# Optimization experiments

Measured on AMD Instinct MI355X. Metric: run time of the kernel, lower is better.

## Reference

```python
import jax, jax.numpy as jnp
import numpy as np

TEMPERATURE = 0.1
NUM_CLASSES = 100
BATCH = 4096
DIM = 128


def setup_inputs() -> dict:
    key = jax.random.key(0)
    k1, k2, k3 = jax.random.split(key, 3)
    centers1 = jax.random.normal(k1, (NUM_CLASSES, DIM), dtype=jnp.float32)
    features = jax.random.normal(k2, (BATCH, 2, DIM), dtype=jnp.float32)
    # contrastive features are typically L2-normalized; harmless and realistic
    centers1 = centers1 / jnp.linalg.norm(centers1, axis=-1, keepdims=True)
    features = features / jnp.linalg.norm(features, axis=-1, keepdims=True)
    targets = jax.random.randint(k3, (BATCH,), 0, NUM_CLASSES, dtype=jnp.int64 if jax.config.jax_enable_x64 else jnp.int32)
    return {"centers1": centers1, "features": features, "targets": targets}


def reference(centers1, features, targets):
    C = centers1.shape[0]          # num classes
    B = features.shape[0]          # batch size
    t = TEMPERATURE

    # targets for [view0; view1; class centers] -> [2B + C]
    tgt = jnp.concatenate([targets, targets, jnp.arange(C, dtype=targets.dtype)])
    # per-class count over all 2B+C target entries (eye(C)[targets].sum(0))
    batch_cls_count = jnp.zeros((C,), jnp.float32).at[tgt].add(1.0)

    # positive mask [2B, 2B+C], zero out self-contrast on the diagonal
    mask = (tgt[: 2 * B, None] == tgt[None, :]).astype(jnp.float32)
    idx = jnp.arange(2 * B)
    logits_mask = jnp.ones((2 * B, 2 * B + C), jnp.float32).at[idx, idx].set(0.0)
    mask = mask * logits_mask

    # stack: [view0 (B), view1 (B), centers (C)] -> [2B+C, D]
    feats = jnp.concatenate([features[:, 0], features[:, 1], centers1], axis=0)

    # logits [2B, 2B+C], stable max-subtract (detached max)
    logits = jnp.matmul(feats[: 2 * B], feats.T) / t
    logits = logits - jax.lax.stop_gradient(jnp.max(logits, axis=1, keepdims=True))

    exp_logits = jnp.exp(logits) * logits_mask
    # per-instance class-balanced weight, minus mask (as in original)
    per_ins_weight = batch_cls_count[tgt][None, :] - mask  # [2B, 2B+C] via broadcast
    exp_logits_sum = jnp.sum(exp_logits / per_ins_weight, axis=1, keepdims=True)

    log_prob = logits - jnp.log(exp_logits_sum)
    mean_log_prob_pos = jnp.sum(mask * log_prob, axis=1) / jnp.sum(mask, axis=1)
    loss = -mean_log_prob_pos
    return loss.reshape(2, B).mean()
```

## Files before the change

kernel.cpp:

```cpp
#include <hip/hip_runtime.h>
#include <math.h>

constexpr int B_   = 4096;
constexpr int C_   = 100;
constexpr int D_   = 128;
constexpr int TWOB = 8192;
constexpr int NJ   = 8292;
constexpr int NJP  = 8320;
constexpr float LOG2E10 = 14.4269504089f;
constexpr float LN2     = 0.6931471805599453f;

typedef __attribute__((ext_vector_type(8))) short short8;
typedef __attribute__((ext_vector_type(4))) float f32x4;


__device__ __forceinline__ const float* feat_row(const float* __restrict__ centers,
                                                 const float* __restrict__ features,
                                                 int idx) {
  if (idx < B_)   return features + (size_t)idx * (2 * D_);
  if (idx < TWOB) return features + (size_t)(idx - B_) * (2 * D_) + D_;
  return centers + (size_t)(idx - TWOB) * D_;
}

__device__ __forceinline__ unsigned short f2bf(float x) {
  unsigned int u = __float_as_uint(x);
  unsigned int r = (u + 0x7FFFu + ((u >> 16) & 1u)) >> 16;
  return (unsigned short)r;
}

__device__ __forceinline__ float bf2f(short s) {
  return __uint_as_float(((unsigned int)(unsigned short)s) << 16);
}

__global__ __launch_bounds__(256)
void tgt_count_kernel(const int* __restrict__ targets, int* __restrict__ cnt,
                      int* __restrict__ tgtAll) {
  int i = blockIdx.x * 256 + threadIdx.x;
  if (i >= NJP) return;
  int jt = (i < B_) ? targets[i]
         : (i < TWOB ? targets[i - B_] : (i < NJ ? i - TWOB : -9));
  tgtAll[i] = jt;
  if (i < B_) atomicAdd(&cnt[jt], 1);
}

__global__ __launch_bounds__(256)
void prep_kernel(const float* __restrict__ centers, const float* __restrict__ features,
                 const int* __restrict__ tgtAll, const int* __restrict__ cnt,
                 unsigned short* __restrict__ fbB, unsigned short* __restrict__ fbA,
                 float4* __restrict__ tbl) {
  int gidx = blockIdx.x * 256 + threadIdx.x;
  if (gidx >= NJP * 32) return;
  int row = gidx >> 5;
  int q   = gidx & 31;
  float4 v = make_float4(0.f, 0.f, 0.f, 0.f);
  if (row < NJ) v = *(const float4*)(feat_row(centers, features, row) + q * 4);
  ushort4 o;
  o.x = f2bf(v.x); o.y = f2bf(v.y); o.z = f2bf(v.z); o.w = f2bf(v.w);
  *(ushort4*)&fbB[(size_t)row * 128 + q * 4] = o;
  if (row < TWOB) {
    ushort4 a;
    a.x = f2bf(v.x * LOG2E10); a.y = f2bf(v.y * LOG2E10);
    a.z = f2bf(v.z * LOG2E10); a.w = f2bf(v.w * LOG2E10);
    *(ushort4*)&fbA[(size_t)row * 128 + q * 4] = a;
  }
  if (q == 0) {
    int jt = tgtAll[row];
    float r0 = 0.f, r1 = 0.f;
    if (jt >= 0) {
      float b = (float)(2 * cnt[jt] + 1);
      r0 = 1.f / b;
      r1 = 1.f / (b - 1.f);
    }
    tbl[row] = make_float4(__int_as_float(jt), r0, r1, 0.f);
  }
}

__global__ __launch_bounds__(256) __attribute__((amdgpu_waves_per_eu(2, 2)))
void bal_mfma(const unsigned short* __restrict__ fbA, const unsigned short* __restrict__ fbB,
              const float4* __restrict__ tbl, float* __restrict__ Eacc,
              float* __restrict__ Sacc) {
  const int t     = threadIdx.x;
  const int lane  = t & 63;
  const int w     = t >> 6;
  const int id    = blockIdx.x;
  const int strip = id & 15;
  const int isup  = id >> 4;
  const int rbase = isup * 256 + w * 64;
  const int lr    = lane & 15;
  const int lh    = lane >> 4;

  const int q0 = strip * 32 + (strip < 8 ? strip : 8);
  const int q1 = q0 + 32 + (strip < 8 ? 1 : 0);

  short8 af[4][4];
  #pragma unroll
  for (int ks = 0; ks < 4; ++ks)
    #pragma unroll
    for (int m = 0; m < 4; ++m)
      af[ks][m] = *(const short8*)&fbA[(size_t)(rbase + m * 16 + lr) * 128 + (ks * 4 + lh) * 8];

  int ti[4][4];
  #pragma unroll
  for (int m = 0; m < 4; ++m)
    #pragma unroll
    for (int g = 0; g < 4; ++g)
      ti[m][g] = __float_as_int(tbl[rbase + m * 16 + lh * 4 + g].x);

  float ep[4][4], ma[4][4];
  #pragma unroll
  for (int m = 0; m < 4; ++m)
    #pragma unroll
    for (int g = 0; g < 4; ++g) { ep[m][g] = 0.f; ma[m][g] = 0.f; }

  short8 bA[4], bB[4];
  float4 tA, tB;

  auto loadQ = [&](int jq, short8 (&b)[4], float4& tb) {
    int jb = jq * 16;
    tb = tbl[jb + lr];
    #pragma unroll
    for (int ks = 0; ks < 4; ++ks)
      b[ks] = *(const short8*)&fbB[(size_t)(jb + lr) * 128 + (ks * 4 + lh) * 8];
  };

  auto computeQ = [&](short8 (&b)[4], float4& tb) {
    f32x4 acc[4];
    #pragma unroll
    for (int m = 0; m < 4; ++m) acc[m] = (f32x4){0.f, 0.f, 0.f, 0.f};
    #pragma unroll
    for (int ks = 0; ks < 4; ++ks)
      #pragma unroll
      for (int m = 0; m < 4; ++m)
        acc[m] = __builtin_amdgcn_mfma_f32_16x16x32_bf16(af[ks][m], b[ks], acc[m], 0, 0, 0);
    int   jtq = __float_as_int(tb.x);
    float r0q = tb.y, r1q = tb.z;
    #pragma unroll
    for (int m = 0; m < 4; ++m)
      #pragma unroll
      for (int g = 0; g < 4; ++g) {
        float a = acc[m][g];
        float e = __builtin_amdgcn_exp2f(a);
        bool eq = (ti[m][g] == jtq);
        ep[m][g] = fmaf(e, eq ? r1q : r0q, ep[m][g]);
        ma[m][g] += eq ? a : 0.f;
      }
  };

  int jq = q0;
  loadQ(q0, bA, tA);
  while (jq + 2 <= q1) {
    loadQ(jq + 1, bB, tB);
    computeQ(bA, tA);
    if (jq + 2 < q1) loadQ(jq + 2, bA, tA);
    computeQ(bB, tB);
    jq += 2;
  }
  if (jq < q1) computeQ(bA, tA);

  #pragma unroll
  for (int mk = 1; mk <= 8; mk <<= 1)
    #pragma unroll
    for (int m = 0; m < 4; ++m)
      #pragma unroll
      for (int g = 0; g < 4; ++g) {
        ep[m][g] += __shfl_xor(ep[m][g], mk, 64);
        ma[m][g] += __shfl_xor(ma[m][g], mk, 64);
      }
  if (lr == 0) {
    #pragma unroll
    for (int m = 0; m < 4; ++m)
      #pragma unroll
      for (int g = 0; g < 4; ++g) {
        int i = rbase + m * 16 + lh * 4 + g;
        atomicAdd(&Eacc[i], ep[m][g]);
        atomicAdd(&Sacc[i], ma[m][g]);
      }
  }
}

__global__ __launch_bounds__(256)
void bal_final(const unsigned short* __restrict__ fbA, const unsigned short* __restrict__ fbB,
               const float4* __restrict__ tbl,
               const float* __restrict__ Eacc, const float* __restrict__ Sacc,
               float* __restrict__ out) {
  int t    = threadIdx.x;
  int row  = blockIdx.x * 64 + (t >> 2);
  int part = t & 3;
  const unsigned short* pa = fbA + (size_t)row * 128 + part * 32;
  const unsigned short* pb = fbB + (size_t)row * 128 + part * 32;
  float4 tb = tbl[row];

  float sA = 0.f;
  #pragma unroll
  for (int q = 0; q < 4; ++q) {
    short8 va = *(const short8*)&pa[q * 8];
    short8 vb = *(const short8*)&pb[q * 8];
    #pragma unroll
    for (int d = 0; d < 8; ++d)
      sA = fmaf(bf2f(va[d]), bf2f(vb[d]), sA);
  }
  sA += __shfl_xor(sA, 1, 64);
  sA += __shfl_xor(sA, 2, 64);

  float r1 = tb.z;
  float ep = Eacc[row] - __builtin_amdgcn_exp2f(sA) * r1;
  float ma = LN2 * (Sacc[row] - sA);
  float li = ma * r1 - logf(ep);
  float local = -li * (1.f / (8192.f * 4.f));

  #pragma unroll
  for (int mk = 1; mk < 64; mk <<= 1) local += __shfl_xor(local, mk, 64);
  if ((t & 63) == 0) atomicAdd(out, local);
}

extern "C" void kernel_launch(void* const* d_in, const int* in_sizes, int n_in,
                              void* d_out, int out_size, void* d_ws, size_t ws_size,
                              hipStream_t stream) {
  const float* centers  = (const float*)d_in[0];
  const float* features = (const float*)d_in[1];
  const int*   targets  = (const int*)d_in[2];

  char* ws = (char*)d_ws;
  int*            cnt    = (int*)ws;
  float*          Eacc   = (float*)(ws + 512);
  float*          Sacc   = (float*)(ws + 33280);
  int*            tgtAll = (int*)(ws + 66048);
  float4*         tbl    = (float4*)(ws + 99328);
  unsigned short* fbB    = (unsigned short*)(ws + 232448);
  unsigned short* fbA    = (unsigned short*)(ws + 2362368);
  float* out = (float*)d_out;

  hipMemsetAsync(ws, 0, 66048, stream);
  hipMemsetAsync(d_out, 0, sizeof(float), stream);
  tgt_count_kernel<<<(NJP + 255) / 256, 256, 0, stream>>>(targets, cnt, tgtAll);
  prep_kernel<<<(NJP * 32 + 255) / 256, 256, 0, stream>>>(centers, features, tgtAll, cnt,
                                                          fbB, fbA, tbl);
  bal_mfma<<<512, 256, 0, stream>>>(fbA, fbB, tbl, Eacc, Sacc);
  bal_final<<<TWOB / 64, 256, 0, stream>>>(fbA, fbB, tbl, Eacc, Sacc, out);
}
```

Baseline: 120.6 us.

## Replace atomics and memsets with per-strip partials and single-block reductions

After: 214.0 us. 1.78x slower.

```diff
diff --git a/kernel.cpp b/kernel.cpp
--- a/kernel.cpp
+++ b/kernel.cpp
@@ -3,7 +3,6 @@
 
 constexpr int B_   = 4096;
 constexpr int C_   = 100;
-constexpr int D_   = 128;
 constexpr int TWOB = 8192;
 constexpr int NJ   = 8292;
 constexpr int NJP  = 8320;
@@ -17,9 +16,9 @@
 __device__ __forceinline__ const float* feat_row(const float* __restrict__ centers,
                                                  const float* __restrict__ features,
                                                  int idx) {
-  if (idx < B_)   return features + (size_t)idx * (2 * D_);
-  if (idx < TWOB) return features + (size_t)(idx - B_) * (2 * D_) + D_;
-  return centers + (size_t)(idx - TWOB) * D_;
+  if (idx < B_)   return features + (size_t)idx * 256;
+  if (idx < TWOB) return features + (size_t)(idx - B_) * 256 + 128;
+  return centers + (size_t)(idx - TWOB) * 128;
 }
 
 __device__ __forceinline__ unsigned short f2bf(float x) {
@@ -32,15 +31,21 @@
   return __uint_as_float(((unsigned int)(unsigned short)s) << 16);
 }
 
-__global__ __launch_bounds__(256)
+__global__ __launch_bounds__(1024)
 void tgt_count_kernel(const int* __restrict__ targets, int* __restrict__ cnt,
                       int* __restrict__ tgtAll) {
-  int i = blockIdx.x * 256 + threadIdx.x;
-  if (i >= NJP) return;
-  int jt = (i < B_) ? targets[i]
-         : (i < TWOB ? targets[i - B_] : (i < NJ ? i - TWOB : -9));
-  tgtAll[i] = jt;
-  if (i < B_) atomicAdd(&cnt[jt], 1);
+  __shared__ int h[128];
+  int t = threadIdx.x;
+  if (t < 128) h[t] = 0;
+  __syncthreads();
+  for (int i = t; i < NJP; i += 1024) {
+    int jt = (i < B_) ? targets[i]
+           : (i < TWOB ? targets[i - B_] : (i < NJ ? i - TWOB : -9));
+    tgtAll[i] = jt;
+    if (i < B_) atomicAdd(&h[jt], 1);
+  }
+  __syncthreads();
+  if (t < 128) cnt[t] = h[t];
 }
 
 __global__ __launch_bounds__(256)
@@ -75,40 +80,40 @@
   }
 }
 
-__global__ __launch_bounds__(256) __attribute__((amdgpu_waves_per_eu(2, 2)))
+__global__ __launch_bounds__(256, 4)
 void bal_mfma(const unsigned short* __restrict__ fbA, const unsigned short* __restrict__ fbB,
-              const float4* __restrict__ tbl, float* __restrict__ Eacc,
-              float* __restrict__ Sacc) {
+              const float4* __restrict__ tbl,
+              float* __restrict__ Epart, float* __restrict__ Spart) {
   const int t     = threadIdx.x;
   const int lane  = t & 63;
   const int w     = t >> 6;
   const int id    = blockIdx.x;
   const int strip = id & 15;
   const int isup  = id >> 4;
-  const int rbase = isup * 256 + w * 64;
+  const int rbase = isup * 128 + w * 32;
   const int lr    = lane & 15;
   const int lh    = lane >> 4;
 
   const int q0 = strip * 32 + (strip < 8 ? strip : 8);
   const int q1 = q0 + 32 + (strip < 8 ? 1 : 0);
 
-  short8 af[4][4];
+  short8 af[4][2];
   #pragma unroll
   for (int ks = 0; ks < 4; ++ks)
     #pragma unroll
-    for (int m = 0; m < 4; ++m)
+    for (int m = 0; m < 2; ++m)
       af[ks][m] = *(const short8*)&fbA[(size_t)(rbase + m * 16 + lr) * 128 + (ks * 4 + lh) * 8];
 
-  int ti[4][4];
-  #pragma unroll
-  for (int m = 0; m < 4; ++m)
+  int ti[2][4];
+  #pragma unroll
+  for (int m = 0; m < 2; ++m)
     #pragma unroll
     for (int g = 0; g < 4; ++g)
       ti[m][g] = __float_as_int(tbl[rbase + m * 16 + lh * 4 + g].x);
 
-  float ep[4][4], ma[4][4];
-  #pragma unroll
-  for (int m = 0; m < 4; ++m)
+  float ep[2][4], ma[2][4];
+  #pragma unroll
+  for (int m = 0; m < 2; ++m)
     #pragma unroll
     for (int g = 0; g < 4; ++g) { ep[m][g] = 0.f; ma[m][g] = 0.f; }
 
@@ -123,44 +128,60 @@
       b[ks] = *(const short8*)&fbB[(size_t)(jb + lr) * 128 + (ks * 4 + lh) * 8];
   };
 
-  auto computeQ = [&](short8 (&b)[4], float4& tb) {
-    f32x4 acc[4];
-    #pragma unroll
-    for (int m = 0; m < 4; ++m) acc[m] = (f32x4){0.f, 0.f, 0.f, 0.f};
+  auto computeQ = [&](int jq, short8 (&b)[4], float4& tb) {
+    const int jb = jq * 16;
+    f32x4 acc[2];
+    #pragma unroll
+    for (int m = 0; m < 2; ++m) acc[m] = (f32x4){0.f, 0.f, 0.f, 0.f};
     #pragma unroll
     for (int ks = 0; ks < 4; ++ks)
       #pragma unroll
-      for (int m = 0; m < 4; ++m)
+      for (int m = 0; m < 2; ++m)
         acc[m] = __builtin_amdgcn_mfma_f32_16x16x32_bf16(af[ks][m], b[ks], acc[m], 0, 0, 0);
-    int   jtq = __float_as_int(tb.x);
-    float r0q = tb.y, r1q = tb.z;
-    #pragma unroll
-    for (int m = 0; m < 4; ++m)
-      #pragma unroll
-      for (int g = 0; g < 4; ++g) {
-        float a = acc[m][g];
-        float e = __builtin_amdgcn_exp2f(a);
-        bool eq = (ti[m][g] == jtq);
-        ep[m][g] = fmaf(e, eq ? r1q : r0q, ep[m][g]);
-        ma[m][g] += eq ? a : 0.f;
-      }
+    const int   jtq = __float_as_int(tb.x);
+    const float r0q = tb.y, r1q = tb.z;
+    if ((unsigned)(jb - rbase) < 32u) {
+      #pragma unroll
+      for (int m = 0; m < 2; ++m)
+        #pragma unroll
+        for (int g = 0; g < 4; ++g) {
+          float a = acc[m][g];
+          float e = __builtin_amdgcn_exp2f(a);
+          bool eq   = (ti[m][g] == jtq);
+          bool diag = (jb + lr) == (rbase + m * 16 + lh * 4 + g);
+          float r = diag ? 0.f : (eq ? r1q : r0q);
+          ep[m][g] = fmaf(e, r, ep[m][g]);
+          ma[m][g] += (eq && !diag) ? a : 0.f;
+        }
+    } else {
+      #pragma unroll
+      for (int m = 0; m < 2; ++m)
+        #pragma unroll
+        for (int g = 0; g < 4; ++g) {
+          float a = acc[m][g];
+          float e = __builtin_amdgcn_exp2f(a);
+          bool eq = (ti[m][g] == jtq);
+          ep[m][g] = fmaf(e, eq ? r1q : r0q, ep[m][g]);
+          ma[m][g] += eq ? a : 0.f;
+        }
+    }
   };
 
   int jq = q0;
   loadQ(q0, bA, tA);
   while (jq + 2 <= q1) {
     loadQ(jq + 1, bB, tB);
-    computeQ(bA, tA);
+    computeQ(jq, bA, tA);
     if (jq + 2 < q1) loadQ(jq + 2, bA, tA);
-    computeQ(bB, tB);
+    computeQ(jq + 1, bB, tB);
     jq += 2;
   }
-  if (jq < q1) computeQ(bA, tA);
+  if (jq < q1) computeQ(jq, bA, tA);
 
   #pragma unroll
   for (int mk = 1; mk <= 8; mk <<= 1)
     #pragma unroll
-    for (int m = 0; m < 4; ++m)
+    for (int m = 0; m < 2; ++m)
       #pragma unroll
       for (int g = 0; g < 4; ++g) {
         ep[m][g] += __shfl_xor(ep[m][g], mk, 64);
@@ -168,49 +189,44 @@
       }
   if (lr == 0) {
     #pragma unroll
-    for (int m = 0; m < 4; ++m)
+    for (int m = 0; m < 2; ++m)
       #pragma unroll
       for (int g = 0; g < 4; ++g) {
         int i = rbase + m * 16 + lh * 4 + g;
-        atomicAdd(&Eacc[i], ep[m][g]);
-        atomicAdd(&Sacc[i], ma[m][g]);
+        Epart[strip * TWOB + i] = ep[m][g];
+        Spart[strip * TWOB + i] = ma[m][g];
       }
   }
 }
 
-__global__ __launch_bounds__(256)
-void bal_final(const unsigned short* __restrict__ fbA, const unsigned short* __restrict__ fbB,
-               const float4* __restrict__ tbl,
-               const float* __restrict__ Eacc, const float* __restrict__ Sacc,
+__global__ __launch_bounds__(1024)
+void bal_final(const float4* __restrict__ tbl,
+               const float* __restrict__ Epart, const float* __restrict__ Spart,
                float* __restrict__ out) {
-  int t    = threadIdx.x;
-  int row  = blockIdx.x * 64 + (t >> 2);
-  int part = t & 3;
-  const unsigned short* pa = fbA + (size_t)row * 128 + part * 32;
-  const unsigned short* pb = fbB + (size_t)row * 128 + part * 32;
-  float4 tb = tbl[row];
-
-  float sA = 0.f;
-  #pragma unroll
-  for (int q = 0; q < 4; ++q) {
-    short8 va = *(const short8*)&pa[q * 8];
-    short8 vb = *(const short8*)&pb[q * 8];
-    #pragma unroll
-    for (int d = 0; d < 8; ++d)
-      sA = fmaf(bf2f(va[d]), bf2f(vb[d]), sA);
-  }
-  sA += __shfl_xor(sA, 1, 64);
-  sA += __shfl_xor(sA, 2, 64);
-
-  float r1 = tb.z;
-  float ep = Eacc[row] - __builtin_amdgcn_exp2f(sA) * r1;
-  float ma = LN2 * (Sacc[row] - sA);
-  float li = ma * r1 - logf(ep);
-  float local = -li * (1.f / (8192.f * 4.f));
-
+  int t = threadIdx.x;
+  float local = 0.f;
+  for (int k = 0; k < 8; ++k) {
+    int row = t + k * 1024;
+    float E = 0.f, S = 0.f;
+    #pragma unroll
+    for (int s = 0; s < 16; ++s) {
+      E += Epart[s * TWOB + row];
+      S += Spart[s * TWOB + row];
+    }
+    float r1 = tbl[row].z;
+    local += LN2 * S * r1 - logf(E);
+  }
   #pragma unroll
   for (int mk = 1; mk < 64; mk <<= 1) local += __shfl_xor(local, mk, 64);
-  if ((t & 63) == 0) atomicAdd(out, local);
+  __shared__ float red[16];
+  if ((t & 63) == 0) red[t >> 6] = local;
+  __syncthreads();
+  if (t == 0) {
+    float s = 0.f;
+    #pragma unroll
+    for (int k = 0; k < 16; ++k) s += red[k];
+    out[0] = -s / (float)TWOB;
+  }
 }
 
 extern "C" void kernel_launch(void* const* d_in, const int* in_sizes, int n_in,
@@ -222,19 +238,17 @@
 
   char* ws = (char*)d_ws;
   int*            cnt    = (int*)ws;
-  float*          Eacc   = (float*)(ws + 512);
-  float*          Sacc   = (float*)(ws + 33280);
-  int*            tgtAll = (int*)(ws + 66048);
-  float4*         tbl    = (float4*)(ws + 99328);
-  unsigned short* fbB    = (unsigned short*)(ws + 232448);
-  unsigned short* fbA    = (unsigned short*)(ws + 2362368);
+  float*          Epart  = (float*)(ws + 512);
+  float*          Spart  = (float*)(ws + 524800);
+  float4*         tbl    = (float4*)(ws + 1049088);
+  int*            tgtAll = (int*)(ws + 1182208);
+  unsigned short* fbB    = (unsigned short*)(ws + 1215488);
+  unsigned short* fbA    = (unsigned short*)(ws + 3345408);
   float* out = (float*)d_out;
 
-  hipMemsetAsync(ws, 0, 66048, stream);
-  hipMemsetAsync(d_out, 0, sizeof(float), stream);
-  tgt_count_kernel<<<(NJP + 255) / 256, 256, 0, stream>>>(targets, cnt, tgtAll);
+  tgt_count_kernel<<<1, 1024, 0, stream>>>(targets, cnt, tgtAll);
   prep_kernel<<<(NJP * 32 + 255) / 256, 256, 0, stream>>>(centers, features, tgtAll, cnt,
                                                           fbB, fbA, tbl);
-  bal_mfma<<<512, 256, 0, stream>>>(fbA, fbB, tbl, Eacc, Sacc);
-  bal_final<<<TWOB / 64, 256, 0, stream>>>(fbA, fbB, tbl, Eacc, Sacc, out);
-}
+  bal_mfma<<<1024, 256, 0, stream>>>(fbA, fbB, tbl, Epart, Spart);
+  bal_final<<<1, 1024, 0, stream>>>(tbl, Epart, Spart, out);
+}
```
